# Performance work log

Hardware: AMD Instinct MI355X
Metric: run time of the kernel (lower is better)

Reference implementation:

```python
import jax, jax.numpy as jnp
import numpy as np

MUL = 256            # multiplicity per irrep in node_feat_irreps = 256x0e+256x1o+256x2e
N_NODES = 65536


def _split_node(node_feats):
    # node_feats layout (e3nn order): [256x0e | 256x1o | 256x2e] = [256 | 768 | 1280]
    x0 = node_feats[:, :MUL]                          # [N, 256]
    x1 = node_feats[:, MUL:4 * MUL].reshape(-1, MUL, 3)   # [N, 256, 3]
    x2 = node_feats[:, 4 * MUL:].reshape(-1, MUL, 5)      # [N, 256, 5]
    return x0, x1, x2


def setup_inputs() -> dict:
    key = jax.random.key(0)
    ks = jax.random.split(key, 8)
    node_feats = jax.random.normal(ks[0], (N_NODES, 9 * MUL), jnp.float32)
    charges = jax.random.normal(ks[1], (N_NODES, 9), jnp.float32)  # 1x0e+1x1o+1x2e
    W_lin0 = jax.random.normal(ks[2], (MUL, MUL), jnp.float32)
    W_lin1 = jax.random.normal(ks[3], (MUL, MUL), jnp.float32)
    W_lin2 = jax.random.normal(ks[4], (MUL, MUL), jnp.float32)
    W_tp0 = jax.random.normal(ks[5], (MUL,), jnp.float32)  # uvw weight [256,1,1] squeezed
    W_tp1 = jax.random.normal(ks[6], (MUL,), jnp.float32)
    W_tp2 = jax.random.normal(ks[7], (MUL,), jnp.float32)
    return dict(node_feats=node_feats, charges=charges,
                W_lin0=W_lin0, W_lin1=W_lin1, W_lin2=W_lin2,
                W_tp0=W_tp0, W_tp1=W_tp1, W_tp2=W_tp2)


def reference(node_feats, charges, W_lin0, W_lin1, W_lin2, W_tp0, W_tp1, W_tp2):
    x0, x1, x2 = _split_node(node_feats)
    c0 = charges[:, 0]        # [N]    0e
    c1 = charges[:, 1:4]      # [N,3]  1o
    c2 = charges[:, 4:9]      # [N,5]  2e

    # o3.Linear: block-diagonal per irrep, weight shared over m, scaled 1/sqrt(fan_in)
    lin_norm = 1.0 / np.sqrt(MUL)
    y0 = (x0 @ W_lin0) * lin_norm                                   # [N,256]
    y1 = jnp.einsum('zui,uv->zvi', x1, W_lin1) * lin_norm           # [N,256,3]
    y2 = jnp.einsum('zui,uv->zvi', x2, W_lin2) * lin_norm           # [N,256,5]

    # FullyConnectedTensorProduct -> 1x0e.
    # wigner_3j(l,l,0)[i,j] = delta_ij / sqrt(2l+1); path norm: 1/sqrt(sum fans) = 1/sqrt(3*MUL)
    alpha = 1.0 / np.sqrt(3.0 * MUL)
    p0 = jnp.einsum('zu,u->z', y0, W_tp0) * c0
    p1 = jnp.einsum('zui,u,zi->z', y1, W_tp1, c1) / np.sqrt(3.0)
    p2 = jnp.einsum('zui,u,zi->z', y2, W_tp2, c2) / np.sqrt(5.0)

    energy = alpha * (p0 + p1 + p2)   # [N] (already squeezed: single 0e channel)
    return energy
```

## Files before the change

kernel.cpp:

```cpp
#include <hip/hip_runtime.h>
#include <math.h>

#define MULC 256
#define ROWF 2304

typedef float f32x4 __attribute__((ext_vector_type(4)));

__global__ __launch_bounds__(64) void build_wfull_kernel(
    const float* __restrict__ Wl0, const float* __restrict__ Wl1,
    const float* __restrict__ Wl2, const float* __restrict__ Wt0,
    const float* __restrict__ Wt1, const float* __restrict__ Wt2,
    float* __restrict__ wfull) {
  const int b    = blockIdx.x;
  const int mat  = b >> 8;
  const int u    = b & 255;
  const int lane = threadIdx.x;

  const float* __restrict__ Wl = (mat == 0) ? Wl0 : (mat == 1) ? Wl1 : Wl2;
  const float* __restrict__ Wt = (mat == 0) ? Wt0 : (mat == 1) ? Wt1 : Wt2;

  float s = 0.f;
#pragma unroll
  for (int t = 0; t < 4; ++t) {
    const int v = lane + 64 * t;
    s = fmaf(Wl[u * MULC + v], Wt[v], s);
  }
#pragma unroll
  for (int off = 32; off > 0; off >>= 1) s += __shfl_down(s, off, 64);

  if (lane == 0) {
    const float base = 0.0625f / sqrtf(768.0f);
    if (mat == 0) {
      wfull[u] = s * base;
    } else if (mat == 1) {
      const float sv = s * base * (1.0f / sqrtf(3.0f));
#pragma unroll
      for (int i = 0; i < 3; ++i) wfull[256 + u * 3 + i] = sv;
    } else {
      const float sv = s * base * (1.0f / sqrtf(5.0f));
#pragma unroll
      for (int i = 0; i < 5; ++i) wfull[1024 + u * 5 + i] = sv;
    }
  }
}

__global__ __launch_bounds__(256) void energy_kernel(
    const float* __restrict__ x, const float* __restrict__ charges,
    const float* __restrict__ wfull, float* __restrict__ out,
    int n_rows, int n_waves) {
  const int lane = threadIdx.x & 63;
  const int wave = (int)((blockIdx.x * blockDim.x + threadIdx.x) >> 6);

  f32x4 w4[9];
  int cpack[9];
#pragma unroll
  for (int j = 0; j < 9; ++j) {
    const int f = lane + 64 * j;
    w4[j] = ((const f32x4*)wfull)[f];
    int p = 0;
#pragma unroll
    for (int m = 0; m < 4; ++m) {
      const int e = 4 * f + m;
      int c;
      if (e < 256)       c = 0;
      else if (e < 1024) c = 1 + (e - 256) % 3;
      else               c = 4 + (e - 1024) % 5;
      p |= (c * 4) << (8 * m);
    }
    cpack[j] = p;
  }

  if (wave >= n_rows) return;

  float chv = 0.f;
  if (lane < 9) chv = charges[(size_t)wave * 9 + lane];

  for (int z = wave; z < n_rows; z += n_waves) {
    const int chvi = __float_as_int(chv);
    const float c0 = __int_as_float(__builtin_amdgcn_readfirstlane(chvi));

    const int zn = z + n_waves;
    float chv_next = 0.f;
    if (zn < n_rows && lane < 9) chv_next = charges[(size_t)zn * 9 + lane];

    const f32x4* __restrict__ xr = (const f32x4*)(x + (size_t)z * ROWF);
    float acc = 0.f;

    {
      const f32x4 v = __builtin_nontemporal_load(&xr[lane]);
      acc = fmaf(v.x, w4[0].x * c0, acc);
      acc = fmaf(v.y, w4[0].y * c0, acc);
      acc = fmaf(v.z, w4[0].z * c0, acc);
      acc = fmaf(v.w, w4[0].w * c0, acc);
    }
#pragma unroll
    for (int j = 1; j < 4; ++j) {
      const f32x4 v = __builtin_nontemporal_load(&xr[lane + 64 * j]);
      const int p = cpack[j];
      const float ca = __int_as_float(__builtin_amdgcn_ds_bpermute(p & 0xff, chvi));
      const float cb = __int_as_float(__builtin_amdgcn_ds_bpermute((p >> 8) & 0xff, chvi));
      const float cc = __int_as_float(__builtin_amdgcn_ds_bpermute((p >> 16) & 0xff, chvi));
      acc = fmaf(v.x, w4[j].x * ca, acc);
      acc = fmaf(v.y, w4[j].y * cb, acc);
      acc = fmaf(v.z, w4[j].z * cc, acc);
      acc = fmaf(v.w, w4[j].w * ca, acc);
    }
#pragma unroll
    for (int j = 4; j < 9; ++j) {
      const f32x4 v = __builtin_nontemporal_load(&xr[lane + 64 * j]);
      const int p = cpack[j];
      const float ca = __int_as_float(__builtin_amdgcn_ds_bpermute(p & 0xff, chvi));
      const float cb = __int_as_float(__builtin_amdgcn_ds_bpermute((p >> 8) & 0xff, chvi));
      const float cc = __int_as_float(__builtin_amdgcn_ds_bpermute((p >> 16) & 0xff, chvi));
      const float cd = __int_as_float(__builtin_amdgcn_ds_bpermute((p >> 24) & 0xff, chvi));
      acc = fmaf(v.x, w4[j].x * ca, acc);
      acc = fmaf(v.y, w4[j].y * cb, acc);
      acc = fmaf(v.z, w4[j].z * cc, acc);
      acc = fmaf(v.w, w4[j].w * cd, acc);
    }

#pragma unroll
    for (int off = 32; off > 0; off >>= 1) acc += __shfl_down(acc, off, 64);
    if (lane == 0) out[z] = acc;

    chv = chv_next;
  }
}

extern "C" void kernel_launch(void* const* d_in, const int* in_sizes, int n_in,
                              void* d_out, int out_size, void* d_ws, size_t ws_size,
                              hipStream_t stream) {
  const float* node_feats = (const float*)d_in[0];
  const float* charges    = (const float*)d_in[1];
  const float* W_lin0     = (const float*)d_in[2];
  const float* W_lin1     = (const float*)d_in[3];
  const float* W_lin2     = (const float*)d_in[4];
  const float* W_tp0      = (const float*)d_in[5];
  const float* W_tp1      = (const float*)d_in[6];
  const float* W_tp2      = (const float*)d_in[7];
  float* out   = (float*)d_out;
  float* wfull = (float*)d_ws;

  const int n_rows = in_sizes[0] / ROWF;

  build_wfull_kernel<<<3 * 256, 64, 0, stream>>>(W_lin0, W_lin1, W_lin2,
                                                 W_tp0, W_tp1, W_tp2, wfull);

  const int blocks  = 4096;
  const int n_waves = blocks * (256 / 64);
  energy_kernel<<<blocks, 256, 0, stream>>>(node_feats, charges, wfull, out,
                                            n_rows, n_waves);
}
```

Before: 731.4 us.

## Accumulate per-charge-component partial sums and process two rows per wave iteration

Each lane now keeps nine per-component accumulators (one for 0e, three for 1o, five for 2e) and applies the charges once at the end. This cuts the charge broadcasts from 32 to 8 per row and removes the per-element weight*charge multiplies. The loop also handles two rows per iteration with interleaved reductions, which raises memory-level parallelism. The cost is more registers and the loss of the charge prefetch for the next row, since charges are now loaded inside the iteration.

```diff
diff --git a/kernel.cpp b/kernel.cpp
--- a/kernel.cpp
+++ b/kernel.cpp
@@ -44,6 +44,50 @@
   }
 }
 
+__device__ __forceinline__ float row_partial(
+    const f32x4* __restrict__ xr, int lane, const f32x4* w4,
+    const int* bp1, const int* bp2, int chvi) {
+  float a0 = 0.f;
+  float a1[3] = {0.f, 0.f, 0.f};
+  float a2[5] = {0.f, 0.f, 0.f, 0.f, 0.f};
+
+  {
+    const f32x4 v = __builtin_nontemporal_load(&xr[lane]);
+    a0 = fmaf(v.x, w4[0].x, a0);
+    a0 = fmaf(v.y, w4[0].y, a0);
+    a0 = fmaf(v.z, w4[0].z, a0);
+    a0 = fmaf(v.w, w4[0].w, a0);
+  }
+#pragma unroll
+  for (int j = 1; j < 4; ++j) {
+    const f32x4 v = __builtin_nontemporal_load(&xr[lane + 64 * j]);
+    { const int s = (j - 1) % 3; a1[s] = fmaf(v.x, w4[j].x, a1[s]); }
+    { const int s = (j    ) % 3; a1[s] = fmaf(v.y, w4[j].y, a1[s]); }
+    { const int s = (j + 1) % 3; a1[s] = fmaf(v.z, w4[j].z, a1[s]); }
+    { const int s = (j + 2) % 3; a1[s] = fmaf(v.w, w4[j].w, a1[s]); }
+  }
+#pragma unroll
+  for (int j = 4; j < 9; ++j) {
+    const f32x4 v = __builtin_nontemporal_load(&xr[lane + 64 * j]);
+    { const int s = (j - 4) % 5; a2[s] = fmaf(v.x, w4[j].x, a2[s]); }
+    { const int s = (j - 3) % 5; a2[s] = fmaf(v.y, w4[j].y, a2[s]); }
+    { const int s = (j - 2) % 5; a2[s] = fmaf(v.z, w4[j].z, a2[s]); }
+    { const int s = (j - 1) % 5; a2[s] = fmaf(v.w, w4[j].w, a2[s]); }
+  }
+
+  const float c0 = __int_as_float(__builtin_amdgcn_readfirstlane(chvi));
+  float t = a0 * c0;
+#pragma unroll
+  for (int s = 0; s < 3; ++s)
+    t = fmaf(a1[s],
+             __int_as_float(__builtin_amdgcn_ds_bpermute(bp1[s], chvi)), t);
+#pragma unroll
+  for (int s = 0; s < 5; ++s)
+    t = fmaf(a2[s],
+             __int_as_float(__builtin_amdgcn_ds_bpermute(bp2[s], chvi)), t);
+  return t;
+}
+
 __global__ __launch_bounds__(256) void energy_kernel(
     const float* __restrict__ x, const float* __restrict__ charges,
     const float* __restrict__ wfull, float* __restrict__ out,
@@ -52,78 +96,49 @@
   const int wave = (int)((blockIdx.x * blockDim.x + threadIdx.x) >> 6);
 
   f32x4 w4[9];
-  int cpack[9];
 #pragma unroll
-  for (int j = 0; j < 9; ++j) {
-    const int f = lane + 64 * j;
-    w4[j] = ((const f32x4*)wfull)[f];
-    int p = 0;
+  for (int j = 0; j < 9; ++j) w4[j] = ((const f32x4*)wfull)[lane + 64 * j];
+
+  int bp1[3], bp2[5];
+  {
+    const int r3 = lane % 3;
+    const int r5 = (4 * lane) % 5;
 #pragma unroll
-    for (int m = 0; m < 4; ++m) {
-      const int e = 4 * f + m;
-      int c;
-      if (e < 256)       c = 0;
-      else if (e < 1024) c = 1 + (e - 256) % 3;
-      else               c = 4 + (e - 1024) % 5;
-      p |= (c * 4) << (8 * m);
-    }
-    cpack[j] = p;
+    for (int s = 0; s < 3; ++s) bp1[s] = 4 * (1 + (s + r3) % 3);
+#pragma unroll
+    for (int s = 0; s < 5; ++s) bp2[s] = 4 * (4 + (s + r5) % 5);
   }
 
   if (wave >= n_rows) return;
 
-  float chv = 0.f;
-  if (lane < 9) chv = charges[(size_t)wave * 9 + lane];
+  for (int z = wave; z < n_rows; z += 2 * n_waves) {
+    const int zB = z + n_waves;
+    const bool hasB = (zB < n_rows);
 
-  for (int z = wave; z < n_rows; z += n_waves) {
-    const int chvi = __float_as_int(chv);
-    const float c0 = __int_as_float(__builtin_amdgcn_readfirstlane(chvi));
+    float chvA = 0.f, chvB = 0.f;
+    if (lane < 9) {
+      chvA = charges[(size_t)z * 9 + lane];
+      if (hasB) chvB = charges[(size_t)zB * 9 + lane];
+    }
 
-    const int zn = z + n_waves;
-    float chv_next = 0.f;
-    if (zn < n_rows && lane < 9) chv_next = charges[(size_t)zn * 9 + lane];
+    const f32x4* __restrict__ xrA = (const f32x4*)(x + (size_t)z * ROWF);
+    float tA = row_partial(xrA, lane, w4, bp1, bp2, __float_as_int(chvA));
 
-    const f32x4* __restrict__ xr = (const f32x4*)(x + (size_t)z * ROWF);
-    float acc = 0.f;
-
-    {
-      const f32x4 v = __builtin_nontemporal_load(&xr[lane]);
-      acc = fmaf(v.x, w4[0].x * c0, acc);
-      acc = fmaf(v.y, w4[0].y * c0, acc);
-      acc = fmaf(v.z, w4[0].z * c0, acc);
-      acc = fmaf(v.w, w4[0].w * c0, acc);
-    }
-#pragma unroll
-    for (int j = 1; j < 4; ++j) {
-      const f32x4 v = __builtin_nontemporal_load(&xr[lane + 64 * j]);
-      const int p = cpack[j];
-      const float ca = __int_as_float(__builtin_amdgcn_ds_bpermute(p & 0xff, chvi));
-      const float cb = __int_as_float(__builtin_amdgcn_ds_bpermute((p >> 8) & 0xff, chvi));
-      const float cc = __int_as_float(__builtin_amdgcn_ds_bpermute((p >> 16) & 0xff, chvi));
-      acc = fmaf(v.x, w4[j].x * ca, acc);
-      acc = fmaf(v.y, w4[j].y * cb, acc);
-      acc = fmaf(v.z, w4[j].z * cc, acc);
-      acc = fmaf(v.w, w4[j].w * ca, acc);
-    }
-#pragma unroll
-    for (int j = 4; j < 9; ++j) {
-      const f32x4 v = __builtin_nontemporal_load(&xr[lane + 64 * j]);
-      const int p = cpack[j];
-      const float ca = __int_as_float(__builtin_amdgcn_ds_bpermute(p & 0xff, chvi));
-      const float cb = __int_as_float(__builtin_amdgcn_ds_bpermute((p >> 8) & 0xff, chvi));
-      const float cc = __int_as_float(__builtin_amdgcn_ds_bpermute((p >> 16) & 0xff, chvi));
-      const float cd = __int_as_float(__builtin_amdgcn_ds_bpermute((p >> 24) & 0xff, chvi));
-      acc = fmaf(v.x, w4[j].x * ca, acc);
-      acc = fmaf(v.y, w4[j].y * cb, acc);
-      acc = fmaf(v.z, w4[j].z * cc, acc);
-      acc = fmaf(v.w, w4[j].w * cd, acc);
+    float tB = 0.f;
+    if (hasB) {
+      const f32x4* __restrict__ xrB = (const f32x4*)(x + (size_t)zB * ROWF);
+      tB = row_partial(xrB, lane, w4, bp1, bp2, __float_as_int(chvB));
     }
 
 #pragma unroll
-    for (int off = 32; off > 0; off >>= 1) acc += __shfl_down(acc, off, 64);
-    if (lane == 0) out[z] = acc;
-
-    chv = chv_next;
+    for (int off = 32; off > 0; off >>= 1) {
+      tA += __shfl_down(tA, off, 64);
+      tB += __shfl_down(tB, off, 64);
+    }
+    if (lane == 0) {
+      out[z] = tA;
+      if (hasB) out[zB] = tB;
+    }
   }
 }
 
```

Result: no change. 731.4 us (+0.0%).
